# Kernel tuning notes

Measured on AMD Instinct MI355X. Metric: run time of the kernel, lower is better.

The kernel has to match this reference:

```python
import jax, jax.numpy as jnp
import numpy as np

N = 50000
E = 300000
D_IN = 256
D_OUT = 256


def setup_inputs() -> dict:
    key = jax.random.key(0)
    ks = jax.random.split(key, 9)
    obj_vecs = jax.random.normal(ks[0], (N, D_IN), dtype=jnp.float32)
    rel_vecs = jax.random.normal(ks[1], (N, D_IN), dtype=jnp.float32)
    edge_index = jax.random.randint(ks[2], (E, 2), 0, N, dtype=jnp.int64)
    s = 1.0 / np.sqrt(D_IN)
    # SAGEConv params: lin_l (applied to aggregated neighbors, with bias),
    # lin_r (applied to root/self features, no bias). One pair per conv.
    W_l_obj = jax.random.uniform(ks[3], (D_OUT, D_IN), minval=-s, maxval=s, dtype=jnp.float32)
    b_l_obj = jax.random.uniform(ks[4], (D_OUT,), minval=-s, maxval=s, dtype=jnp.float32)
    W_r_obj = jax.random.uniform(ks[5], (D_OUT, D_IN), minval=-s, maxval=s, dtype=jnp.float32)
    W_l_rel = jax.random.uniform(ks[6], (D_OUT, D_IN), minval=-s, maxval=s, dtype=jnp.float32)
    b_l_rel = jax.random.uniform(ks[7], (D_OUT,), minval=-s, maxval=s, dtype=jnp.float32)
    W_r_rel = jax.random.uniform(ks[8], (D_OUT, D_IN), minval=-s, maxval=s, dtype=jnp.float32)
    return {"obj_vecs": obj_vecs, "rel_vecs": rel_vecs, "edge_index": edge_index,
            "W_l_obj": W_l_obj, "b_l_obj": b_l_obj, "W_r_obj": W_r_obj,
            "W_l_rel": W_l_rel, "b_l_rel": b_l_rel, "W_r_rel": W_r_rel}


def _sage_conv(x, src, dst, W_l, b_l, W_r):
    # mean aggregation of source-node features at destination nodes
    msg = x[src]                                             # [E, D_IN] gather
    summed = jax.ops.segment_sum(msg, dst, num_segments=N)   # [N, D_IN]
    cnt = jax.ops.segment_sum(jnp.ones((src.shape[0],), x.dtype), dst, num_segments=N)
    agg = summed / jnp.maximum(cnt, 1.0)[:, None]
    # out = lin_l(agg) + lin_r(x)
    return agg @ W_l.T + b_l + x @ W_r.T


def reference(obj_vecs, rel_vecs, edge_index,
              W_l_obj, b_l_obj, W_r_obj, W_l_rel, b_l_rel, W_r_rel):
    # module transposes [E,2] -> [2,E]; PyG: messages flow src=row0 -> dst=row1
    src = edge_index[:, 0]
    dst = edge_index[:, 1]
    obj_out = _sage_conv(obj_vecs, src, dst, W_l_obj, b_l_obj, W_r_obj)
    rel_out = _sage_conv(rel_vecs, src, dst, W_l_rel, b_l_rel, W_r_rel)
    return (obj_out, rel_out)
```

## Files before the change

kernel.cpp:

```cpp
#include <hip/hip_runtime.h>

#define N_NODES 50000
#define N_EDGES 300000
#define DFEAT 256
#define KCAT 512
#define MT 32
#define APAD 8
#define AROW (KCAT + APAD)
#define SCAN_NBLK ((N_NODES + 255) / 256)

typedef __attribute__((ext_vector_type(8))) short bf16x8;
typedef __attribute__((ext_vector_type(4))) float f32x4;

__device__ __forceinline__ unsigned short f2bf(float f) {
    union { float f; unsigned int u; } c; c.f = f;
    unsigned int r = c.u + 0x7FFF + ((c.u >> 16) & 1);
    return (unsigned short)(r >> 16);
}

__global__ void k_zero(int4* __restrict__ p, int n4) {
    int i = blockIdx.x * blockDim.x + threadIdx.x;
    int stride = gridDim.x * blockDim.x;
    for (; i < n4; i += stride) p[i] = make_int4(0, 0, 0, 0);
}

__global__ void k_hist(const int* __restrict__ ei, int* __restrict__ cnt, int E) {
    int e = blockIdx.x * blockDim.x + threadIdx.x;
    if (e < E) {
        unsigned d = (unsigned)ei[2 * e + 1];
        if (d < (unsigned)N_NODES) atomicAdd(&cnt[d], 1);
    }
}

__global__ void k_scan_a(const int* __restrict__ cnt, int* __restrict__ bsum, int n) {
    int b = blockIdx.x, t = threadIdx.x;
    int i = b * 256 + t;
    int v = (i < n) ? cnt[i] : 0;
    #pragma unroll
    for (int d = 32; d; d >>= 1) v += __shfl_down(v, d, 64);
    __shared__ int ws[4];
    if ((t & 63) == 0) ws[t >> 6] = v;
    __syncthreads();
    if (t == 0) bsum[b] = ws[0] + ws[1] + ws[2] + ws[3];
}

__global__ void k_scan_b(const int* __restrict__ bsum, int* __restrict__ bpre,
                         int* __restrict__ off, int nblk, int n) {
    __shared__ int lds[256];
    int t = threadIdx.x;
    int v = (t < nblk) ? bsum[t] : 0;
    lds[t] = v;
    __syncthreads();
    for (int d = 1; d < 256; d <<= 1) {
        int u = (t >= d) ? lds[t - d] : 0;
        __syncthreads();
        lds[t] += u;
        __syncthreads();
    }
    if (t < nblk) bpre[t] = lds[t] - v;
    if (t == 255) off[n] = lds[255];
}

__global__ void k_scan_c(const int* __restrict__ cnt, const int* __restrict__ bpre,
                         int* __restrict__ off, int* __restrict__ cursor, int n) {
    __shared__ int lds[256];
    int b = blockIdx.x, t = threadIdx.x;
    int i = b * 256 + t;
    int v = (i < n) ? cnt[i] : 0;
    lds[t] = v;
    __syncthreads();
    for (int d = 1; d < 256; d <<= 1) {
        int u = (t >= d) ? lds[t - d] : 0;
        __syncthreads();
        lds[t] += u;
        __syncthreads();
    }
    if (i < n) {
        int ex = bpre[b] + lds[t] - v;
        off[i] = ex;
        cursor[i] = ex;
    }
}

__global__ void k_scatter(const int* __restrict__ ei, int* __restrict__ cursor,
                          int* __restrict__ srcs, int E) {
    int e = blockIdx.x * blockDim.x + threadIdx.x;
    if (e < E) {
        unsigned s = (unsigned)ei[2 * e];
        unsigned d = (unsigned)ei[2 * e + 1];
        if (d < (unsigned)N_NODES && s < (unsigned)N_NODES) {
            unsigned pos = (unsigned)atomicAdd(&cursor[d], 1);
            if (pos < (unsigned)E) srcs[pos] = (int)s;
        }
    }
}

__global__ void k_wt(const float* __restrict__ Wl, const float* __restrict__ Wr,
                     unsigned short* __restrict__ Wb) {
    int id = blockIdx.x * blockDim.x + threadIdx.x;
    int j    = id & 7;
    int lane = (id >> 3) & 63;
    int frag = id >> 9;
    int nt   = frag & 15;
    int kb   = frag >> 4;
    int k = kb * 32 + (lane >> 4) * 8 + j;
    int n = nt * 16 + (lane & 15);
    float v = (k < 256) ? Wl[n * 256 + k] : Wr[n * 256 + (k - 256)];
    Wb[id] = f2bf(v);
}

__global__ __launch_bounds__(256, 4)
void k_fused(const float* __restrict__ x_obj, const float* __restrict__ x_rel,
             const unsigned short* __restrict__ Wb_obj, const unsigned short* __restrict__ Wb_rel,
             const float* __restrict__ b_obj, const float* __restrict__ b_rel,
             const int* __restrict__ off, const int* __restrict__ srcs,
             float* __restrict__ out, int n) {
    __shared__ unsigned short A[MT][AROW];

    const int tz = blockIdx.y;
    const float* __restrict__ x   = tz ? x_rel  : x_obj;
    const unsigned short* __restrict__ Wb = tz ? Wb_rel : Wb_obj;
    const float* __restrict__ bia = tz ? b_rel  : b_obj;
    float* __restrict__ outp = out + (size_t)tz * (size_t)N_NODES * DFEAT;

    const int t = threadIdx.x;
    const int wave = t >> 6, lane = t & 63;
    const int node0 = blockIdx.x * MT;

    const float4* __restrict__ x4 = (const float4*)x;
    for (int il = wave; il < MT; il += 4) {
        int node = node0 + il;
        float4 accv = make_float4(0.f, 0.f, 0.f, 0.f);
        float4 xv   = make_float4(0.f, 0.f, 0.f, 0.f);
        if (node < n) {
            xv = x4[(size_t)node * 64 + lane];
            int eb = off[node], ee = off[node + 1];
            if (eb < 0) eb = 0;
            if (ee > N_EDGES) ee = N_EDGES;
            if (ee < eb) ee = eb;
            int e = eb;
            for (; e + 3 < ee; e += 4) {
                unsigned s0 = (unsigned)srcs[e],     s1 = (unsigned)srcs[e + 1];
                unsigned s2 = (unsigned)srcs[e + 2], s3 = (unsigned)srcs[e + 3];
                if (s0 >= (unsigned)n) s0 = 0;
                if (s1 >= (unsigned)n) s1 = 0;
                if (s2 >= (unsigned)n) s2 = 0;
                if (s3 >= (unsigned)n) s3 = 0;
                float4 v0 = x4[(size_t)s0 * 64 + lane];
                float4 v1 = x4[(size_t)s1 * 64 + lane];
                float4 v2 = x4[(size_t)s2 * 64 + lane];
                float4 v3 = x4[(size_t)s3 * 64 + lane];
                accv.x += (v0.x + v1.x) + (v2.x + v3.x);
                accv.y += (v0.y + v1.y) + (v2.y + v3.y);
                accv.z += (v0.z + v1.z) + (v2.z + v3.z);
                accv.w += (v0.w + v1.w) + (v2.w + v3.w);
            }
            if (e + 1 < ee) {
                unsigned s0 = (unsigned)srcs[e], s1 = (unsigned)srcs[e + 1];
                if (s0 >= (unsigned)n) s0 = 0;
                if (s1 >= (unsigned)n) s1 = 0;
                float4 v0 = x4[(size_t)s0 * 64 + lane];
                float4 v1 = x4[(size_t)s1 * 64 + lane];
                accv.x += v0.x + v1.x; accv.y += v0.y + v1.y;
                accv.z += v0.z + v1.z; accv.w += v0.w + v1.w;
                e += 2;
            }
            if (e < ee) {
                unsigned s0 = (unsigned)srcs[e];
                if (s0 >= (unsigned)n) s0 = 0;
                float4 v = x4[(size_t)s0 * 64 + lane];
                accv.x += v.x; accv.y += v.y; accv.z += v.z; accv.w += v.w;
            }
            float c = (float)(ee - eb);
            float inv = 1.0f / fmaxf(c, 1.0f);
            accv.x *= inv; accv.y *= inv; accv.z *= inv; accv.w *= inv;
        }
        ushort4 a16 = make_ushort4(f2bf(accv.x), f2bf(accv.y), f2bf(accv.z), f2bf(accv.w));
        ushort4 x16 = make_ushort4(f2bf(xv.x),  f2bf(xv.y),  f2bf(xv.z),  f2bf(xv.w));
        *(ushort4*)&A[il][4 * lane]       = a16;
        *(ushort4*)&A[il][256 + 4 * lane] = x16;
    }
    __syncthreads();

    const int r0  = (wave & 1) * 16;
    const int nt0 = (wave >> 1) * 8;
    const int lq  = lane >> 4;
    const int lm  = lane & 15;

    f32x4 acc[8];
    #pragma unroll
    for (int ct = 0; ct < 8; ct++) {
        float b = bia[(nt0 + ct) * 16 + lm];
        acc[ct] = (f32x4){b, b, b, b};
    }

    const bf16x8* __restrict__ Wb8 = (const bf16x8*)Wb;
    #pragma unroll
    for (int kb = 0; kb < 16; kb++) {
        bf16x8 af = *(const bf16x8*)&A[r0 + lm][kb * 32 + lq * 8];
        #pragma unroll
        for (int ct = 0; ct < 8; ct++) {
            bf16x8 bf = Wb8[(size_t)(kb * 16 + nt0 + ct) * 64 + lane];
            acc[ct] = __builtin_amdgcn_mfma_f32_16x16x32_bf16(af, bf, acc[ct], 0, 0, 0);
        }
    }

    #pragma unroll
    for (int ct = 0; ct < 8; ct++) {
        int col = (nt0 + ct) * 16 + lm;
        #pragma unroll
        for (int r = 0; r < 4; r++) {
            int node = node0 + r0 + lq * 4 + r;
            if (node < n) outp[((size_t)node << 8) + col] = acc[ct][r];
        }
    }
}

extern "C" void kernel_launch(void* const* d_in, const int* in_sizes, int n_in,
                              void* d_out, int out_size, void* d_ws, size_t ws_size,
                              hipStream_t stream) {
    const float* obj  = (const float*)d_in[0];
    const float* rel  = (const float*)d_in[1];
    const int*   ei   = (const int*)d_in[2];
    const float* Wl_o = (const float*)d_in[3];
    const float* bl_o = (const float*)d_in[4];
    const float* Wr_o = (const float*)d_in[5];
    const float* Wl_r = (const float*)d_in[6];
    const float* bl_r = (const float*)d_in[7];
    const float* Wr_r = (const float*)d_in[8];
    float* out = (float*)d_out;

    char* w = (char*)d_ws;
    size_t o = 0;
    auto alloc = [&](size_t b) { size_t r = o; o += (b + 255) & ~(size_t)255; return r; };
    size_t csr_base = o;
    int*            cnt    = (int*)(w + alloc((size_t)N_NODES * 4));
    int*            off    = (int*)(w + alloc((size_t)(N_NODES + 1) * 4));
    int*            cursor = (int*)(w + alloc((size_t)N_NODES * 4));
    int*            srcs   = (int*)(w + alloc((size_t)N_EDGES * 4));
    size_t csr_bytes = o - csr_base;
    int*            bsum   = (int*)(w + alloc(256 * 4));
    int*            bpre   = (int*)(w + alloc(256 * 4));
    unsigned short* Wb_o   = (unsigned short*)(w + alloc((size_t)KCAT * DFEAT * 2));
    unsigned short* Wb_r   = (unsigned short*)(w + alloc((size_t)KCAT * DFEAT * 2));

    int n4 = (int)(csr_bytes / 16);
    k_zero<<<512, 256, 0, stream>>>((int4*)(w + csr_base), n4);
    k_hist<<<(N_EDGES + 255) / 256, 256, 0, stream>>>(ei, cnt, N_EDGES);
    k_scan_a<<<SCAN_NBLK, 256, 0, stream>>>(cnt, bsum, N_NODES);
    k_scan_b<<<1, 256, 0, stream>>>(bsum, bpre, off, SCAN_NBLK, N_NODES);
    k_scan_c<<<SCAN_NBLK, 256, 0, stream>>>(cnt, bpre, off, cursor, N_NODES);
    k_scatter<<<(N_EDGES + 255) / 256, 256, 0, stream>>>(ei, cursor, srcs, N_EDGES);
    k_wt<<<(KCAT * DFEAT) / 256, 256, 0, stream>>>(Wl_o, Wr_o, Wb_o);
    k_wt<<<(KCAT * DFEAT) / 256, 256, 0, stream>>>(Wl_r, Wr_r, Wb_r);

    dim3 g((N_NODES + MT - 1) / MT, 2);
    k_fused<<<g, 256, 0, stream>>>(obj, rel, Wb_o, Wb_r, bl_o, bl_r, off, srcs, out, N_NODES);
}
```

Measured before the change: 349.5 us.

## Fuse CSR prep into persistent kernel and gather bf16-converted features

Replaces the chain of small CSR-build and weight-packing kernels with a single persistent kernel that uses a software grid barrier between phases. The same kernel also converts both feature matrices to bf16 once, and the fused aggregation/GEMM kernel then gathers the bf16 rows, halving the bytes moved per neighbor. This removes launch gaps and reduces gather bandwidth, at the cost of an extra conversion pass and slightly different rounding, since inputs are rounded to bf16 before summation. The grid barrier relies on all prep blocks being co-resident.

```diff
diff --git a/kernel.cpp b/kernel.cpp
--- a/kernel.cpp
+++ b/kernel.cpp
@@ -8,8 +8,12 @@
 #define APAD 8
 #define AROW (KCAT + APAD)
 #define SCAN_NBLK ((N_NODES + 255) / 256)
+#define NB_PREP 304
+#define WT_IDS (KCAT * DFEAT)
+#define CONV4 (N_NODES * DFEAT / 4)
 
 typedef __attribute__((ext_vector_type(8))) short bf16x8;
+typedef __attribute__((ext_vector_type(8))) unsigned short u16x8;
 typedef __attribute__((ext_vector_type(4))) float f32x4;
 
 __device__ __forceinline__ unsigned short f2bf(float f) {
@@ -17,100 +21,138 @@
     unsigned int r = c.u + 0x7FFF + ((c.u >> 16) & 1);
     return (unsigned short)(r >> 16);
 }
-
-__global__ void k_zero(int4* __restrict__ p, int n4) {
-    int i = blockIdx.x * blockDim.x + threadIdx.x;
-    int stride = gridDim.x * blockDim.x;
-    for (; i < n4; i += stride) p[i] = make_int4(0, 0, 0, 0);
-}
-
-__global__ void k_hist(const int* __restrict__ ei, int* __restrict__ cnt, int E) {
-    int e = blockIdx.x * blockDim.x + threadIdx.x;
-    if (e < E) {
+__device__ __forceinline__ float bf2f(unsigned short u) {
+    union { unsigned int i; float f; } c; c.i = ((unsigned int)u) << 16;
+    return c.f;
+}
+
+__global__ void k_bzero(int* __restrict__ bar) {
+    if (threadIdx.x < 16) bar[threadIdx.x] = 0;
+}
+
+__device__ __forceinline__ void gbar(int* bar, int phase) {
+    __syncthreads();
+    if (threadIdx.x == 0) {
+        __threadfence();
+        __hip_atomic_fetch_add(bar, 1, __ATOMIC_ACQ_REL, __HIP_MEMORY_SCOPE_AGENT);
+        int target = phase * (int)gridDim.x;
+        while (__hip_atomic_load(bar, __ATOMIC_ACQUIRE, __HIP_MEMORY_SCOPE_AGENT) < target) {
+            __builtin_amdgcn_s_sleep(2);
+        }
+    }
+    __syncthreads();
+}
+
+__global__ __launch_bounds__(256, 2)
+void k_prep(const int* __restrict__ ei,
+            const float* __restrict__ Wl_o, const float* __restrict__ Wr_o,
+            const float* __restrict__ Wl_r, const float* __restrict__ Wr_r,
+            const float* __restrict__ x_obj, const float* __restrict__ x_rel,
+            int* __restrict__ cnt, int* __restrict__ off, int* __restrict__ cursor,
+            int* __restrict__ srcs, int* __restrict__ bsum, int* __restrict__ bpre,
+            unsigned short* __restrict__ Wb_o, unsigned short* __restrict__ Wb_r,
+            ushort4* __restrict__ xb_o, ushort4* __restrict__ xb_r,
+            int* __restrict__ bar) {
+    __shared__ int slds[256];
+    const int bid = blockIdx.x, t = threadIdx.x;
+    const int g = bid * 256 + t;
+    const int gs = (int)gridDim.x * 256;
+
+    for (int i = g; i < N_NODES; i += gs) cnt[i] = 0;
+
+    for (int id = g; id < 2 * WT_IDS; id += gs) {
+        int tz = id >> 17;
+        int l  = id & (WT_IDS - 1);
+        int j    = l & 7;
+        int lane = (l >> 3) & 63;
+        int frag = l >> 9;
+        int nt   = frag & 15;
+        int kb   = frag >> 4;
+        int k  = kb * 32 + (lane >> 4) * 8 + j;
+        int nn = nt * 16 + (lane & 15);
+        const float* Wl = tz ? Wl_r : Wl_o;
+        const float* Wr = tz ? Wr_r : Wr_o;
+        float v = (k < 256) ? Wl[nn * 256 + k] : Wr[nn * 256 + (k - 256)];
+        (tz ? Wb_r : Wb_o)[l] = f2bf(v);
+    }
+
+    const float4* xo4 = (const float4*)x_obj;
+    const float4* xr4 = (const float4*)x_rel;
+    for (int id = g; id < 2 * CONV4; id += gs) {
+        int tz = (id >= CONV4);
+        int e4 = tz ? id - CONV4 : id;
+        float4 v = tz ? xr4[e4] : xo4[e4];
+        ushort4 o = make_ushort4(f2bf(v.x), f2bf(v.y), f2bf(v.z), f2bf(v.w));
+        (tz ? xb_r : xb_o)[e4] = o;
+    }
+    gbar(bar, 1);
+
+    for (int e = g; e < N_EDGES; e += gs) {
         unsigned d = (unsigned)ei[2 * e + 1];
         if (d < (unsigned)N_NODES) atomicAdd(&cnt[d], 1);
     }
-}
-
-__global__ void k_scan_a(const int* __restrict__ cnt, int* __restrict__ bsum, int n) {
-    int b = blockIdx.x, t = threadIdx.x;
-    int i = b * 256 + t;
-    int v = (i < n) ? cnt[i] : 0;
-    #pragma unroll
-    for (int d = 32; d; d >>= 1) v += __shfl_down(v, d, 64);
-    __shared__ int ws[4];
-    if ((t & 63) == 0) ws[t >> 6] = v;
-    __syncthreads();
-    if (t == 0) bsum[b] = ws[0] + ws[1] + ws[2] + ws[3];
-}
-
-__global__ void k_scan_b(const int* __restrict__ bsum, int* __restrict__ bpre,
-                         int* __restrict__ off, int nblk, int n) {
-    __shared__ int lds[256];
-    int t = threadIdx.x;
-    int v = (t < nblk) ? bsum[t] : 0;
-    lds[t] = v;
-    __syncthreads();
-    for (int d = 1; d < 256; d <<= 1) {
-        int u = (t >= d) ? lds[t - d] : 0;
-        __syncthreads();
-        lds[t] += u;
-        __syncthreads();
-    }
-    if (t < nblk) bpre[t] = lds[t] - v;
-    if (t == 255) off[n] = lds[255];
-}
-
-__global__ void k_scan_c(const int* __restrict__ cnt, const int* __restrict__ bpre,
-                         int* __restrict__ off, int* __restrict__ cursor, int n) {
-    __shared__ int lds[256];
-    int b = blockIdx.x, t = threadIdx.x;
-    int i = b * 256 + t;
-    int v = (i < n) ? cnt[i] : 0;
-    lds[t] = v;
-    __syncthreads();
-    for (int d = 1; d < 256; d <<= 1) {
-        int u = (t >= d) ? lds[t - d] : 0;
-        __syncthreads();
-        lds[t] += u;
-        __syncthreads();
-    }
-    if (i < n) {
-        int ex = bpre[b] + lds[t] - v;
-        off[i] = ex;
-        cursor[i] = ex;
-    }
-}
-
-__global__ void k_scatter(const int* __restrict__ ei, int* __restrict__ cursor,
-                          int* __restrict__ srcs, int E) {
-    int e = blockIdx.x * blockDim.x + threadIdx.x;
-    if (e < E) {
+    gbar(bar, 2);
+
+    if (bid < SCAN_NBLK) {
+        int i = bid * 256 + t;
+        int v = (i < N_NODES) ? cnt[i] : 0;
+        #pragma unroll
+        for (int d = 32; d; d >>= 1) v += __shfl_down(v, d, 64);
+        if ((t & 63) == 0) slds[t >> 6] = v;
+        __syncthreads();
+        if (t == 0) bsum[bid] = slds[0] + slds[1] + slds[2] + slds[3];
+        __syncthreads();
+    }
+    gbar(bar, 3);
+
+    if (bid == 0) {
+        int v = (t < SCAN_NBLK) ? bsum[t] : 0;
+        slds[t] = v;
+        __syncthreads();
+        for (int d = 1; d < 256; d <<= 1) {
+            int u = (t >= d) ? slds[t - d] : 0;
+            __syncthreads();
+            slds[t] += u;
+            __syncthreads();
+        }
+        if (t < SCAN_NBLK) bpre[t] = slds[t] - v;
+        if (t == 255) off[N_NODES] = slds[255];
+        __syncthreads();
+    }
+    gbar(bar, 4);
+
+    if (bid < SCAN_NBLK) {
+        int i = bid * 256 + t;
+        int v = (i < N_NODES) ? cnt[i] : 0;
+        slds[t] = v;
+        __syncthreads();
+        for (int d = 1; d < 256; d <<= 1) {
+            int u = (t >= d) ? slds[t - d] : 0;
+            __syncthreads();
+            slds[t] += u;
+            __syncthreads();
+        }
+        if (i < N_NODES) {
+            int ex = bpre[bid] + slds[t] - v;
+            off[i] = ex;
+            cursor[i] = ex;
+        }
+        __syncthreads();
+    }
+    gbar(bar, 5);
+
+    for (int e = g; e < N_EDGES; e += gs) {
         unsigned s = (unsigned)ei[2 * e];
         unsigned d = (unsigned)ei[2 * e + 1];
         if (d < (unsigned)N_NODES && s < (unsigned)N_NODES) {
             unsigned pos = (unsigned)atomicAdd(&cursor[d], 1);
-            if (pos < (unsigned)E) srcs[pos] = (int)s;
-        }
-    }
-}
-
-__global__ void k_wt(const float* __restrict__ Wl, const float* __restrict__ Wr,
-                     unsigned short* __restrict__ Wb) {
-    int id = blockIdx.x * blockDim.x + threadIdx.x;
-    int j    = id & 7;
-    int lane = (id >> 3) & 63;
-    int frag = id >> 9;
-    int nt   = frag & 15;
-    int kb   = frag >> 4;
-    int k = kb * 32 + (lane >> 4) * 8 + j;
-    int n = nt * 16 + (lane & 15);
-    float v = (k < 256) ? Wl[n * 256 + k] : Wr[n * 256 + (k - 256)];
-    Wb[id] = f2bf(v);
+            if (pos < (unsigned)N_EDGES) srcs[pos] = (int)s;
+        }
+    }
 }
 
 __global__ __launch_bounds__(256, 4)
-void k_fused(const float* __restrict__ x_obj, const float* __restrict__ x_rel,
+void k_fused(const unsigned short* __restrict__ xb_obj, const unsigned short* __restrict__ xb_rel,
              const unsigned short* __restrict__ Wb_obj, const unsigned short* __restrict__ Wb_rel,
              const float* __restrict__ b_obj, const float* __restrict__ b_rel,
              const int* __restrict__ off, const int* __restrict__ srcs,
@@ -118,70 +160,74 @@
     __shared__ unsigned short A[MT][AROW];
 
     const int tz = blockIdx.y;
-    const float* __restrict__ x   = tz ? x_rel  : x_obj;
+    const unsigned short* __restrict__ xb = tz ? xb_rel : xb_obj;
     const unsigned short* __restrict__ Wb = tz ? Wb_rel : Wb_obj;
-    const float* __restrict__ bia = tz ? b_rel  : b_obj;
+    const float* __restrict__ bia = tz ? b_rel : b_obj;
     float* __restrict__ outp = out + (size_t)tz * (size_t)N_NODES * DFEAT;
 
     const int t = threadIdx.x;
-    const int wave = t >> 6, lane = t & 63;
     const int node0 = blockIdx.x * MT;
 
-    const float4* __restrict__ x4 = (const float4*)x;
-    for (int il = wave; il < MT; il += 4) {
+    const int half = t >> 5;
+    const int l32  = t & 31;
+    const u16x8* __restrict__ xb8 = (const u16x8*)xb;
+
+    for (int q = 0; q < 4; q++) {
+        int il = half * 4 + q;
         int node = node0 + il;
-        float4 accv = make_float4(0.f, 0.f, 0.f, 0.f);
-        float4 xv   = make_float4(0.f, 0.f, 0.f, 0.f);
+        float a[8] = {0.f, 0.f, 0.f, 0.f, 0.f, 0.f, 0.f, 0.f};
+        u16x8 xv = (u16x8){0, 0, 0, 0, 0, 0, 0, 0};
+        int eb = 0, ee = 0;
         if (node < n) {
-            xv = x4[(size_t)node * 64 + lane];
-            int eb = off[node], ee = off[node + 1];
+            xv = xb8[(size_t)node * 32 + l32];
+            eb = off[node]; ee = off[node + 1];
             if (eb < 0) eb = 0;
             if (ee > N_EDGES) ee = N_EDGES;
             if (ee < eb) ee = eb;
-            int e = eb;
-            for (; e + 3 < ee; e += 4) {
-                unsigned s0 = (unsigned)srcs[e],     s1 = (unsigned)srcs[e + 1];
-                unsigned s2 = (unsigned)srcs[e + 2], s3 = (unsigned)srcs[e + 3];
-                if (s0 >= (unsigned)n) s0 = 0;
-                if (s1 >= (unsigned)n) s1 = 0;
-                if (s2 >= (unsigned)n) s2 = 0;
-                if (s3 >= (unsigned)n) s3 = 0;
-                float4 v0 = x4[(size_t)s0 * 64 + lane];
-                float4 v1 = x4[(size_t)s1 * 64 + lane];
-                float4 v2 = x4[(size_t)s2 * 64 + lane];
-                float4 v3 = x4[(size_t)s3 * 64 + lane];
-                accv.x += (v0.x + v1.x) + (v2.x + v3.x);
-                accv.y += (v0.y + v1.y) + (v2.y + v3.y);
-                accv.z += (v0.z + v1.z) + (v2.z + v3.z);
-                accv.w += (v0.w + v1.w) + (v2.w + v3.w);
-            }
-            if (e + 1 < ee) {
-                unsigned s0 = (unsigned)srcs[e], s1 = (unsigned)srcs[e + 1];
-                if (s0 >= (unsigned)n) s0 = 0;
-                if (s1 >= (unsigned)n) s1 = 0;
-                float4 v0 = x4[(size_t)s0 * 64 + lane];
-                float4 v1 = x4[(size_t)s1 * 64 + lane];
-                accv.x += v0.x + v1.x; accv.y += v0.y + v1.y;
-                accv.z += v0.z + v1.z; accv.w += v0.w + v1.w;
-                e += 2;
-            }
-            if (e < ee) {
-                unsigned s0 = (unsigned)srcs[e];
-                if (s0 >= (unsigned)n) s0 = 0;
-                float4 v = x4[(size_t)s0 * 64 + lane];
-                accv.x += v.x; accv.y += v.y; accv.z += v.z; accv.w += v.w;
-            }
-            float c = (float)(ee - eb);
-            float inv = 1.0f / fmaxf(c, 1.0f);
-            accv.x *= inv; accv.y *= inv; accv.z *= inv; accv.w *= inv;
-        }
-        ushort4 a16 = make_ushort4(f2bf(accv.x), f2bf(accv.y), f2bf(accv.z), f2bf(accv.w));
-        ushort4 x16 = make_ushort4(f2bf(xv.x),  f2bf(xv.y),  f2bf(xv.z),  f2bf(xv.w));
-        *(ushort4*)&A[il][4 * lane]       = a16;
-        *(ushort4*)&A[il][256 + 4 * lane] = x16;
+        }
+        int e = eb;
+        for (; e + 3 < ee; e += 4) {
+            unsigned s0 = (unsigned)srcs[e],     s1 = (unsigned)srcs[e + 1];
+            unsigned s2 = (unsigned)srcs[e + 2], s3 = (unsigned)srcs[e + 3];
+            if (s0 >= (unsigned)n) s0 = 0;
+            if (s1 >= (unsigned)n) s1 = 0;
+            if (s2 >= (unsigned)n) s2 = 0;
+            if (s3 >= (unsigned)n) s3 = 0;
+            u16x8 v0 = xb8[(size_t)s0 * 32 + l32];
+            u16x8 v1 = xb8[(size_t)s1 * 32 + l32];
+            u16x8 v2 = xb8[(size_t)s2 * 32 + l32];
+            u16x8 v3 = xb8[(size_t)s3 * 32 + l32];
+            #pragma unroll
+            for (int j = 0; j < 8; j++)
+                a[j] += (bf2f(v0[j]) + bf2f(v1[j])) + (bf2f(v2[j]) + bf2f(v3[j]));
+        }
+        if (e + 1 < ee) {
+            unsigned s0 = (unsigned)srcs[e], s1 = (unsigned)srcs[e + 1];
+            if (s0 >= (unsigned)n) s0 = 0;
+            if (s1 >= (unsigned)n) s1 = 0;
+            u16x8 v0 = xb8[(size_t)s0 * 32 + l32];
+            u16x8 v1 = xb8[(size_t)s1 * 32 + l32];
+            #pragma unroll
+            for (int j = 0; j < 8; j++) a[j] += bf2f(v0[j]) + bf2f(v1[j]);
+            e += 2;
+        }
+        if (e < ee) {
+            unsigned s0 = (unsigned)srcs[e];
+            if (s0 >= (unsigned)n) s0 = 0;
+            u16x8 v0 = xb8[(size_t)s0 * 32 + l32];
+            #pragma unroll
+            for (int j = 0; j < 8; j++) a[j] += bf2f(v0[j]);
+        }
+        float inv = 1.0f / fmaxf((float)(ee - eb), 1.0f);
+        u16x8 av;
+        #pragma unroll
+        for (int j = 0; j < 8; j++) av[j] = f2bf(a[j] * inv);
+        *(u16x8*)&A[il][l32 * 8]       = av;
+        *(u16x8*)&A[il][256 + l32 * 8] = xv;
     }
     __syncthreads();
 
+    const int wave = t >> 6, lane = t & 63;
     const int r0  = (wave & 1) * 16;
     const int nt0 = (wave >> 1) * 8;
     const int lq  = lane >> 4;
@@ -233,27 +279,23 @@
     char* w = (char*)d_ws;
     size_t o = 0;
     auto alloc = [&](size_t b) { size_t r = o; o += (b + 255) & ~(size_t)255; return r; };
-    size_t csr_base = o;
     int*            cnt    = (int*)(w + alloc((size_t)N_NODES * 4));
     int*            off    = (int*)(w + alloc((size_t)(N_NODES + 1) * 4));
     int*            cursor = (int*)(w + alloc((size_t)N_NODES * 4));
     int*            srcs   = (int*)(w + alloc((size_t)N_EDGES * 4));
-    size_t csr_bytes = o - csr_base;
     int*            bsum   = (int*)(w + alloc(256 * 4));
     int*            bpre   = (int*)(w + alloc(256 * 4));
+    int*            bar    = (int*)(w + alloc(256));
     unsigned short* Wb_o   = (unsigned short*)(w + alloc((size_t)KCAT * DFEAT * 2));
     unsigned short* Wb_r   = (unsigned short*)(w + alloc((size_t)KCAT * DFEAT * 2));
-
-    int n4 = (int)(csr_bytes / 16);
-    k_zero<<<512, 256, 0, stream>>>((int4*)(w + csr_base), n4);
-    k_hist<<<(N_EDGES + 255) / 256, 256, 0, stream>>>(ei, cnt, N_EDGES);
-    k_scan_a<<<SCAN_NBLK, 256, 0, stream>>>(cnt, bsum, N_NODES);
-    k_scan_b<<<1, 256, 0, stream>>>(bsum, bpre, off, SCAN_NBLK, N_NODES);
-    k_scan_c<<<SCAN_NBLK, 256, 0, stream>>>(cnt, bpre, off, cursor, N_NODES);
-    k_scatter<<<(N_EDGES + 255) / 256, 256, 0, stream>>>(ei, cursor, srcs, N_EDGES);
-    k_wt<<<(KCAT * DFEAT) / 256, 256, 0, stream>>>(Wl_o, Wr_o, Wb_o);
-    k_wt<<<(KCAT * DFEAT) / 256, 256, 0, stream>>>(Wl_r, Wr_r, Wb_r);
-
+    ushort4*        xb_o   = (ushort4*)(w + alloc((size_t)N_NODES * DFEAT * 2));
+    ushort4*        xb_r   = (ushort4*)(w + alloc((size_t)N_NODES * DFEAT * 2));
+
+    k_bzero<<<1, 64, 0, stream>>>(bar);
+    k_prep<<<NB_PREP, 256, 0, stream>>>(ei, Wl_o, Wr_o, Wl_r, Wr_r, obj, rel,
+                                        cnt, off, cursor, srcs, bsum, bpre,
+                                        Wb_o, Wb_r, xb_o, xb_r, bar);
     dim3 g((N_NODES + MT - 1) / MT, 2);
-    k_fused<<<g, 256, 0, stream>>>(obj, rel, Wb_o, Wb_r, bl_o, bl_r, off, srcs, out, N_NODES);
-}
+    k_fused<<<g, 256, 0, stream>>>((const unsigned short*)xb_o, (const unsigned short*)xb_r,
+                                   Wb_o, Wb_r, bl_o, bl_r, off, srcs, out, N_NODES);
+}
```

New measurement: 525.4 us. 50.3% more time.
